# Performance work log

Measured on AMD Instinct MI355X. Metric: run time of the kernel, lower is better.

Reference implementation:

```python
import jax, jax.numpy as jnp
import numpy as np

D_MODEL = 512
NUM_HEADS = 8
DEPTH = D_MODEL // NUM_HEADS


def setup_inputs() -> dict:
    key = jax.random.key(0)
    ks = jax.random.split(key, 12)
    B, S, D = 2, 4096, D_MODEL
    scale = 1.0 / np.sqrt(D)
    return {
        "q": jax.random.normal(ks[0], (B, S, D), jnp.float32),
        "k": jax.random.normal(ks[1], (B, S, D), jnp.float32),
        "v": jax.random.normal(ks[2], (B, S, D), jnp.float32),
        "mask": jnp.zeros((B, 1, 1, S), jnp.float32),
        "wq": jax.random.normal(ks[3], (D, D), jnp.float32) * scale,
        "bq": jnp.zeros((D,), jnp.float32),
        "wk": jax.random.normal(ks[4], (D, D), jnp.float32) * scale,
        "bk": jnp.zeros((D,), jnp.float32),
        "wv": jax.random.normal(ks[5], (D, D), jnp.float32) * scale,
        "bv": jnp.zeros((D,), jnp.float32),
        "wo": jax.random.normal(ks[6], (D, D), jnp.float32) * scale,
        "bo": jnp.zeros((D,), jnp.float32),
    }


def _split_heads(x):
    # [B, S, D] -> [B, H, S, depth]
    B, S, _ = x.shape
    return x.reshape(B, S, NUM_HEADS, DEPTH).transpose(0, 2, 1, 3)


def reference(q, k, v, mask, wq, bq, wk, bk, wv, bv, wo, bo):
    B, S, D = q.shape
    query = _split_heads(q @ wq + bq)   # [B,H,S,d]
    key = _split_heads(k @ wk + bk)
    value = _split_heads(v @ wv + bv)
    # NOTE: original module does NOT scale by 1/sqrt(depth)
    score = jnp.einsum("bhqd,bhkd->bhqk", query, key)
    score = score + mask * -1e9
    attn = jax.nn.softmax(score, axis=-1)
    out = jnp.einsum("bhqk,bhkd->bhqd", attn, value)  # [B,H,S,d]
    out = out.transpose(0, 2, 1, 3).reshape(B, S, D)
    return out @ wo + bo
```

## Files before the change

kernel.cpp:

```cpp
#include <hip/hip_runtime.h>

#define NH   8
#define DH   64
#define NB   2
#define SEQ  4096
#define DM   512
#define MR   (NB * SEQ)
#define LSTR 72
#define LOG2E 1.44269504089f
#define NSPL 2
#define KVS  (SEQ / NSPL)
#define RH   (NB * NH * SEQ)

using f16x8 = __attribute__((ext_vector_type(8))) _Float16;
using f32x4 = __attribute__((ext_vector_type(4))) float;
using h2    = __attribute__((ext_vector_type(2))) _Float16;
#define MFMA16(a, b, c) __builtin_amdgcn_mfma_f32_16x16x32_f16(a, b, c, 0, 0, 0)

#if defined(__has_builtin) && __has_builtin(__builtin_amdgcn_exp2f)
#define EXP2(x) __builtin_amdgcn_exp2f(x)
#else
extern "C" __device__ float __ocml_native_exp2_f32(float);
#define EXP2(x) __ocml_native_exp2_f32(x)
#endif

__device__ __forceinline__ unsigned pk_f16(float a, float b) {
    typedef __fp16 fp16v2 __attribute__((ext_vector_type(2)));
    union { fp16v2 h; unsigned u; } c;
    c.h = __builtin_amdgcn_cvt_pkrtz(a, b);
    return c.u;
}
__device__ __forceinline__ unsigned sel_shfl(unsigned a, unsigned b, int pick, int src) {
    const unsigned va = __shfl(a, src);
    const unsigned vb = __shfl(b, src);
    return pick ? vb : va;
}
__device__ __forceinline__ float m3(float a, float b, float c) {
    return fmaxf(fmaxf(a, b), c);
}
__device__ __forceinline__ float dot2acc(unsigned u, float c) {
#if defined(__has_builtin) && __has_builtin(__builtin_amdgcn_fdot2)
    h2 a = __builtin_bit_cast(h2, u);
    h2 one = {(_Float16)1.f, (_Float16)1.f};
    return __builtin_amdgcn_fdot2(a, one, c, false);
#else
    h2 a = __builtin_bit_cast(h2, u);
    return c + (float)a[0] + (float)a[1];
#endif
}
__device__ __forceinline__ void async16(void* lds, const void* g) {
    __builtin_amdgcn_global_load_lds(
        (__attribute__((address_space(1))) void*)g,
        (__attribute__((address_space(3))) void*)lds, 16, 0, 0);
}

__global__ __launch_bounds__(256) void cvt_w(
    const float* __restrict__ w0, const float* __restrict__ w1,
    const float* __restrict__ w2, const float* __restrict__ w3,
    _Float16* __restrict__ Wt)
{
    __shared__ _Float16 T[64 * LSTR];
    const int z = blockIdx.z;
    const float* W = (z == 0) ? w0 : (z == 1 ? w1 : (z == 2 ? w2 : w3));
    _Float16* out = Wt + (size_t)z * DM * DM;
    const int t = threadIdx.x;
    const int k0 = blockIdx.x * 64, n0 = blockIdx.y * 64;
#pragma unroll
    for (int i = 0; i < 4; ++i) {
        const int kl  = i * 16 + (t >> 4);
        const int nl4 = (t & 15) * 4;
        float4 u = *(const float4*)(W + (size_t)(k0 + kl) * DM + n0 + nl4);
        T[(nl4 + 0) * LSTR + kl] = (_Float16)u.x;
        T[(nl4 + 1) * LSTR + kl] = (_Float16)u.y;
        T[(nl4 + 2) * LSTR + kl] = (_Float16)u.z;
        T[(nl4 + 3) * LSTR + kl] = (_Float16)u.w;
    }
    __syncthreads();
#pragma unroll
    for (int i = 0; i < 2; ++i) {
        const int nl = i * 32 + (t >> 3);
        const int kc = (t & 7) * 8;
        *(uint4*)(out + (size_t)(n0 + nl) * DM + k0 + kc) = *(const uint4*)&T[nl * LSTR + kc];
    }
}

__global__ __launch_bounds__(256) void maskprep(const float* __restrict__ mask,
                                                float* __restrict__ mw)
{
    const int i = blockIdx.x * 256 + threadIdx.x;
    mw[i] = mask[i] * (-1e9f * LOG2E);
}

__global__ __launch_bounds__(256) void cvt_qkv(
    const float* __restrict__ q, const float* __restrict__ k,
    const float* __restrict__ v,
    _Float16* __restrict__ Qo, _Float16* __restrict__ Ko, _Float16* __restrict__ Vo)
{
    const size_t PER = (size_t)MR * DM;
    size_t base = ((size_t)blockIdx.x * 256 + threadIdx.x) * 8;
    const int tz = (int)(base / PER);
    const size_t off = base % PER;
    const float* s = (tz == 0) ? q : (tz == 1 ? k : v);
    _Float16* d    = (tz == 0) ? Qo : (tz == 1 ? Ko : Vo);
    float4 a = *(const float4*)(s + off);
    float4 b = *(const float4*)(s + off + 4);
    uint4 p = make_uint4(pk_f16(a.x, a.y), pk_f16(a.z, a.w),
                         pk_f16(b.x, b.y), pk_f16(b.z, b.w));
    *(uint4*)(d + off) = p;
}

__global__ __launch_bounds__(256) void proj3(
    const _Float16* __restrict__ Qin, const _Float16* __restrict__ Kin,
    const _Float16* __restrict__ Vin, const _Float16* __restrict__ Wt,
    const float* __restrict__ bq, const float* __restrict__ bk,
    const float* __restrict__ bv,
    _Float16* __restrict__ Qo, _Float16* __restrict__ Ko,
    _Float16* __restrict__ VTo)
{
    __shared__ _Float16 Xs[2][128 * 64];
    __shared__ _Float16 Ws[2][64 * 64];

    const int z = blockIdx.z;
    const _Float16* X = (z == 0) ? Qin : (z == 1 ? Kin : Vin);
    const _Float16* W = Wt + (size_t)z * DM * DM;
    const float* bias = (z == 0) ? bq : (z == 1 ? bk : bv);
    const float scale = (z == 0) ? LOG2E : 1.0f;

    const int t = threadIdx.x;
    const int l = t & 63, w = t >> 6;
    const int m = l & 15, g = l >> 4;
    const int ms = m & 7;
    const int row0 = blockIdx.x * 128;
    const int col0 = blockIdx.y * 64;

    int xr[4], xsw[4];
#pragma unroll
    for (int i = 0; i < 4; ++i) {
        const int c = w * 256 + i * 64 + l;
        xr[i]  = c >> 3;
        xsw[i] = ((c & 7) ^ (xr[i] & 7)) * 8;
    }
    int wr[2], wsw[2];
#pragma unroll
    for (int i = 0; i < 2; ++i) {
        const int c = w * 128 + i * 64 + l;
        wr[i]  = c >> 3;
        wsw[i] = ((c & 7) ^ (wr[i] & 7)) * 8;
    }

#pragma unroll
    for (int i = 0; i < 4; ++i)
        async16(&Xs[0][(w * 256 + i * 64) * 8], X + (size_t)(row0 + xr[i]) * DM + xsw[i]);
#pragma unroll
    for (int i = 0; i < 2; ++i)
        async16(&Ws[0][(w * 128 + i * 64) * 8], W + (size_t)(col0 + wr[i]) * DM + wsw[i]);

    f32x4 acc[2][4] = {};

    for (int k0 = 0; k0 < DM; k0 += 64) {
        const int p = (k0 >> 6) & 1;
        __syncthreads();
        if (k0 + 64 < DM) {
            const int kn = k0 + 64;
#pragma unroll
            for (int i = 0; i < 4; ++i)
                async16(&Xs[p ^ 1][(w * 256 + i * 64) * 8],
                        X + (size_t)(row0 + xr[i]) * DM + kn + xsw[i]);
#pragma unroll
            for (int i = 0; i < 2; ++i)
                async16(&Ws[p ^ 1][(w * 128 + i * 64) * 8],
                        W + (size_t)(col0 + wr[i]) * DM + kn + wsw[i]);
        }
#pragma unroll
        for (int kk = 0; kk < 2; ++kk) {
            const int slot = ((kk * 4 + g) ^ ms) * 8;
            f16x8 a0 = *(const f16x8*)&Xs[p][(w * 32 + m) * 64 + slot];
            f16x8 a1 = *(const f16x8*)&Xs[p][(w * 32 + 16 + m) * 64 + slot];
#pragma unroll
            for (int ct = 0; ct < 4; ++ct) {
                f16x8 bf = *(const f16x8*)&Ws[p][(ct * 16 + m) * 64 + slot];
                acc[0][ct] = MFMA16(a0, bf, acc[0][ct]);
                acc[1][ct] = MFMA16(a1, bf, acc[1][ct]);
            }
        }
    }

    float bv4[4];
#pragma unroll
    for (int ct = 0; ct < 4; ++ct) bv4[ct] = bias[col0 + ct * 16 + m];

    if (z == 2) {
        __syncthreads();
        _Float16* T = &Xs[0][0];
#pragma unroll
        for (int rt = 0; rt < 2; ++rt)
#pragma unroll
            for (int reg = 0; reg < 4; ++reg) {
                const int s_l = w * 32 + rt * 16 + g * 4 + reg;
#pragma unroll
                for (int ct = 0; ct < 4; ++ct) {
                    const int d = ct * 16 + m;
                    T[d * 136 + s_l] = (_Float16)(acc[rt][ct][reg] + bv4[ct]);
                }
            }
        __syncthreads();
        const int bb = row0 >> 12;
        const int s0 = row0 & (SEQ - 1);
#pragma unroll
        for (int j = 0; j < 4; ++j) {
            const int c = j * 256 + t;
            const int d = c >> 4;
            const int sc = (c & 15) * 8;
            *(uint4*)(VTo + (((size_t)bb * NH + blockIdx.y) * DH + d) * SEQ + s0 + sc) =
                *(const uint4*)&T[d * 136 + sc];
        }
    } else {
        _Float16* out = (z == 0) ? Qo : Ko;
#pragma unroll
        for (int rt = 0; rt < 2; ++rt)
#pragma unroll
            for (int reg = 0; reg < 4; ++reg) {
                const int row = row0 + w * 32 + rt * 16 + g * 4 + reg;
                const int bb = row >> 12;
                const int s  = row & (SEQ - 1);
#pragma unroll
                for (int ct = 0; ct < 4; ++ct)
                    out[(((size_t)bb * NH + blockIdx.y) * SEQ + s) * DH + ct * 16 + m] =
                        (_Float16)(scale * (acc[rt][ct][reg] + bv4[ct]));
            }
    }
}

__global__ __launch_bounds__(256) void gemm_out(const _Float16* __restrict__ X,
                                                const _Float16* __restrict__ W,
                                                const float* __restrict__ bias,
                                                float* __restrict__ out)
{
    __shared__ _Float16 Xs[2][128 * 64];
    __shared__ _Float16 Ws[2][64 * 64];

    const int t = threadIdx.x;
    const int l = t & 63, w = t >> 6;
    const int m = l & 15, g = l >> 4;
    const int ms = m & 7;
    const int row0 = blockIdx.x * 128;
    const int col0 = blockIdx.y * 64;

    int xr[4], xsw[4];
#pragma unroll
    for (int i = 0; i < 4; ++i) {
        const int c = w * 256 + i * 64 + l;
        xr[i]  = c >> 3;
        xsw[i] = ((c & 7) ^ (xr[i] & 7)) * 8;
    }
    int wr[2], wsw[2];
#pragma unroll
    for (int i = 0; i < 2; ++i) {
        const int c = w * 128 + i * 64 + l;
        wr[i]  = c >> 3;
        wsw[i] = ((c & 7) ^ (wr[i] & 7)) * 8;
    }

#pragma unroll
    for (int i = 0; i < 4; ++i)
        async16(&Xs[0][(w * 256 + i * 64) * 8], X + (size_t)(row0 + xr[i]) * DM + xsw[i]);
#pragma unroll
    for (int i = 0; i < 2; ++i)
        async16(&Ws[0][(w * 128 + i * 64) * 8], W + (size_t)(col0 + wr[i]) * DM + wsw[i]);

    f32x4 acc[2][4] = {};

    for (int k0 = 0; k0 < DM; k0 += 64) {
        const int p = (k0 >> 6) & 1;
        __syncthreads();
        if (k0 + 64 < DM) {
            const int kn = k0 + 64;
#pragma unroll
            for (int i = 0; i < 4; ++i)
                async16(&Xs[p ^ 1][(w * 256 + i * 64) * 8],
                        X + (size_t)(row0 + xr[i]) * DM + kn + xsw[i]);
#pragma unroll
            for (int i = 0; i < 2; ++i)
                async16(&Ws[p ^ 1][(w * 128 + i * 64) * 8],
                        W + (size_t)(col0 + wr[i]) * DM + kn + wsw[i]);
        }
#pragma unroll
        for (int kk = 0; kk < 2; ++kk) {
            const int slot = ((kk * 4 + g) ^ ms) * 8;
            f16x8 a0 = *(const f16x8*)&Xs[p][(w * 32 + m) * 64 + slot];
            f16x8 a1 = *(const f16x8*)&Xs[p][(w * 32 + 16 + m) * 64 + slot];
#pragma unroll
            for (int ct = 0; ct < 4; ++ct) {
                f16x8 bf = *(const f16x8*)&Ws[p][(ct * 16 + m) * 64 + slot];
                acc[0][ct] = MFMA16(a0, bf, acc[0][ct]);
                acc[1][ct] = MFMA16(a1, bf, acc[1][ct]);
            }
        }
    }

    float bv4[4];
#pragma unroll
    for (int ct = 0; ct < 4; ++ct) bv4[ct] = bias[col0 + ct * 16 + m];

#pragma unroll
    for (int rt = 0; rt < 2; ++rt)
#pragma unroll
        for (int reg = 0; reg < 4; ++reg) {
            const int row = row0 + w * 32 + rt * 16 + g * 4 + reg;
#pragma unroll
            for (int ct = 0; ct < 4; ++ct)
                out[(size_t)row * DM + col0 + ct * 16 + m] = acc[rt][ct][reg] + bv4[ct];
        }
}

__global__ __launch_bounds__(256) void flash_mfma(
    const _Float16* __restrict__ Q, const _Float16* __restrict__ K,
    const _Float16* __restrict__ VT, const float* __restrict__ mw,
    _Float16* __restrict__ Op, float* __restrict__ Ml)
{
    __shared__ _Float16 Ks [2][64 * 64];
    __shared__ _Float16 VTs[2][64 * 64];

    const int t = threadIdx.x;
    const int l = t & 63, w = t >> 6;
    const int m = l & 15, g = l >> 4;
    const int bh = blockIdx.y;
    const int b  = bh >> 3;
    const int q0 = blockIdx.x * 128;
    const int z  = blockIdx.z;
    const int kb0 = z * KVS;

    const _Float16* Qh  = Q  + (size_t)bh * SEQ * DH;
    const _Float16* Kh  = K  + (size_t)bh * SEQ * DH;
    const _Float16* VTh = VT + (size_t)bh * DH * SEQ;
    const float* mwb = mw + (size_t)b * SEQ;

    const int c0 = w * 128 + l, c1 = c0 + 64;
    const int r0 = c0 >> 3,     r1 = c1 >> 3;
    const int cl0 = (c0 & 7) ^ (r0 & 7), cl1 = (c1 & 7) ^ (r1 & 7);
    const int    gK0 = r0 * DH + cl0 * 8, gK1 = r1 * DH + cl1 * 8;
    const size_t gV0 = (size_t)r0 * SEQ + cl0 * 8, gV1 = (size_t)r1 * SEQ + cl1 * 8;
    const int ldsA = w * 1024, ldsB = ldsA + 512;

    async16(&Ks[0][ldsA], Kh + (size_t)kb0 * DH + gK0);
    async16(&Ks[0][ldsB], Kh + (size_t)kb0 * DH + gK1);
    async16(&VTs[0][ldsA], VTh + kb0 + gV0);
    async16(&VTs[0][ldsB], VTh + kb0 + gV1);

    f16x8 qf[2][2];
#pragma unroll
    for (int h = 0; h < 2; ++h)
#pragma unroll
        for (int kk = 0; kk < 2; ++kk)
            qf[h][kk] = *(const f16x8*)(Qh + (size_t)(q0 + w * 32 + h * 16 + m) * DH +
                                        kk * 32 + g * 8);

    float m_r[2] = {-INFINITY, -INFINITY}, l_r[2] = {0.f, 0.f};
    f32x4 oacc[2][4] = {};

    const int srcA = m + (((g * 2) & 3) << 4);
    const int srcB = m + (((g * 2 + 1) & 3) << 4);
    const int pick = g >> 1;
    const int ms = m & 7;

    for (int it = 0; it < KVS / 64; ++it) {
        const int t0 = kb0 + it * 64;
        const int p  = it & 1;
        __syncthreads();

        if (it + 1 < KVS / 64) {
            const int tn = t0 + 64;
            async16(&Ks[p ^ 1][ldsA], Kh + (size_t)tn * DH + gK0);
            async16(&Ks[p ^ 1][ldsB], Kh + (size_t)tn * DH + gK1);
            async16(&VTs[p ^ 1][ldsA], VTh + tn + gV0);
            async16(&VTs[p ^ 1][ldsB], VTh + tn + gV1);
        }

        f32x4 sacc[2][4];
#pragma unroll
        for (int kt = 0; kt < 4; ++kt) {
            const f32x4 mv = *(const f32x4*)&mwb[t0 + kt * 16 + g * 4];
            sacc[0][kt] = mv;
            sacc[1][kt] = mv;
        }
#pragma unroll
        for (int kk = 0; kk < 2; ++kk) {
            const int slot = ((kk * 4 + g) ^ ms) * 8;
#pragma unroll
            for (int kt = 0; kt < 4; ++kt) {
                f16x8 kf = *(const f16x8*)&Ks[p][(kt * 16 + m) * 64 + slot];
                sacc[0][kt] = MFMA16(kf, qf[0][kk], sacc[0][kt]);
                sacc[1][kt] = MFMA16(kf, qf[1][kk], sacc[1][kt]);
            }
        }

        float rmax[2];
#pragma unroll
        for (int h = 0; h < 2; ++h) {
            const float x0 = m3(sacc[h][0][0], sacc[h][0][1], sacc[h][0][2]);
            const float x1 = m3(sacc[h][0][3], sacc[h][1][0], sacc[h][1][1]);
            const float x2 = m3(sacc[h][1][2], sacc[h][1][3], sacc[h][2][0]);
            const float x3 = m3(sacc[h][2][1], sacc[h][2][2], sacc[h][2][3]);
            const float x4 = m3(sacc[h][3][0], sacc[h][3][1], sacc[h][3][2]);
            float r = fmaxf(m3(x0, x1, x2), m3(x3, x4, sacc[h][3][3]));
            r = fmaxf(r, __shfl_xor(r, 16));
            r = fmaxf(r, __shfl_xor(r, 32));
            rmax[h] = r;
        }

        if (!__all(rmax[0] <= m_r[0] + 8.f && rmax[1] <= m_r[1] + 8.f)) {
#pragma unroll
            for (int h = 0; h < 2; ++h) {
                const float mnew  = fmaxf(m_r[h], rmax[h]);
                const float alpha = EXP2(m_r[h] - mnew);
                m_r[h] = mnew;
                l_r[h] *= alpha;
#pragma unroll
                for (int dt = 0; dt < 4; ++dt)
#pragma unroll
                    for (int r = 0; r < 4; ++r) oacc[h][dt][r] *= alpha;
            }
        }

        unsigned pkw[2][4][2];
#pragma unroll
        for (int h = 0; h < 2; ++h) {
            float ps0 = 0.f, ps1 = 0.f;
#pragma unroll
            for (int kt = 0; kt < 4; ++kt) {
                const float p0 = EXP2(sacc[h][kt][0] - m_r[h]);
                const float p1 = EXP2(sacc[h][kt][1] - m_r[h]);
                const float p2 = EXP2(sacc[h][kt][2] - m_r[h]);
                const float p3 = EXP2(sacc[h][kt][3] - m_r[h]);
                pkw[h][kt][0] = pk_f16(p0, p1);
                pkw[h][kt][1] = pk_f16(p2, p3);
                if (kt < 2) {
                    ps0 = dot2acc(pkw[h][kt][0], ps0);
                    ps0 = dot2acc(pkw[h][kt][1], ps0);
                } else {
                    ps1 = dot2acc(pkw[h][kt][0], ps1);
                    ps1 = dot2acc(pkw[h][kt][1], ps1);
                }
            }
            l_r[h] += ps0 + ps1;
        }

#pragma unroll
        for (int kk = 0; kk < 2; ++kk) {
            union { unsigned u[4]; f16x8 h; } pf[2];
#pragma unroll
            for (int h = 0; h < 2; ++h) {
                pf[h].u[0] = sel_shfl(pkw[h][2 * kk][0], pkw[h][2 * kk + 1][0], pick, srcA);
                pf[h].u[1] = sel_shfl(pkw[h][2 * kk][1], pkw[h][2 * kk + 1][1], pick, srcA);
                pf[h].u[2] = sel_shfl(pkw[h][2 * kk][0], pkw[h][2 * kk + 1][0], pick, srcB);
                pf[h].u[3] = sel_shfl(pkw[h][2 * kk][1], pkw[h][2 * kk + 1][1], pick, srcB);
            }
            const int slot = ((kk * 4 + g) ^ ms) * 8;
#pragma unroll
            for (int dt = 0; dt < 4; ++dt) {
                f16x8 vf = *(const f16x8*)&VTs[p][(dt * 16 + m) * 64 + slot];
                oacc[0][dt] = MFMA16(vf, pf[0].h, oacc[0][dt]);
                oacc[1][dt] = MFMA16(vf, pf[1].h, oacc[1][dt]);
            }
        }
    }

#pragma unroll
    for (int h = 0; h < 2; ++h) {
        float lv = l_r[h];
        lv += __shfl_xor(lv, 16);
        lv += __shfl_xor(lv, 32);
        const float inv = 1.0f / lv;
        const int q = q0 + w * 32 + h * 16 + m;
        const size_t rowi = ((size_t)z * NB * NH + bh) * SEQ + q;
        _Float16* Orow = Op + rowi * DH;
#pragma unroll
        for (int dt = 0; dt < 4; ++dt) {
            _Float16 o4[4] = { (_Float16)(oacc[h][dt][0] * inv),
                               (_Float16)(oacc[h][dt][1] * inv),
                               (_Float16)(oacc[h][dt][2] * inv),
                               (_Float16)(oacc[h][dt][3] * inv) };
            *(uint2*)(Orow + dt * 16 + g * 4) = *(const uint2*)o4;
        }
        if (g == 0) ((float2*)Ml)[rowi] = make_float2(m_r[h], lv);
    }
}

__global__ __launch_bounds__(256) void combine(const _Float16* __restrict__ Op,
                                               const float* __restrict__ Ml,
                                               _Float16* __restrict__ O)
{
    const int i = blockIdx.x * 256 + threadIdx.x;
    const int r = i >> 4;
    const int dq = (i & 15) * 4;
    const float2 ml0 = ((const float2*)Ml)[r];
    const float2 ml1 = ((const float2*)Ml)[RH + r];
    const float M = fmaxf(ml0.x, ml1.x);
    float a0 = EXP2(ml0.x - M) * ml0.y;
    float a1 = EXP2(ml1.x - M) * ml1.y;
    const float inv = 1.f / (a0 + a1);
    a0 *= inv; a1 *= inv;
    union { uint2 u; _Float16 h[4]; } v0, v1, o;
    v0.u = *(const uint2*)(Op + (size_t)r * DH + dq);
    v1.u = *(const uint2*)(Op + ((size_t)RH + r) * DH + dq);
#pragma unroll
    for (int j = 0; j < 4; ++j)
        o.h[j] = (_Float16)(a0 * (float)v0.h[j] + a1 * (float)v1.h[j]);
    const int bh = r >> 12, q = r & (SEQ - 1);
    const int b = bh >> 3, h = bh & 7;
    *(uint2*)(O + ((size_t)b * SEQ + q) * DM + h * DH + dq) = o.u;
}

extern "C" void kernel_launch(void* const* d_in, const int* in_sizes, int n_in,
                              void* d_out, int out_size, void* d_ws, size_t ws_size,
                              hipStream_t stream) {
    const float* q    = (const float*)d_in[0];
    const float* k    = (const float*)d_in[1];
    const float* v    = (const float*)d_in[2];
    const float* mask = (const float*)d_in[3];
    const float* wq   = (const float*)d_in[4];
    const float* bq   = (const float*)d_in[5];
    const float* wk   = (const float*)d_in[6];
    const float* bk   = (const float*)d_in[7];
    const float* wv   = (const float*)d_in[8];
    const float* bv   = (const float*)d_in[9];
    const float* wo   = (const float*)d_in[10];
    const float* bo   = (const float*)d_in[11];

    const size_t P8 = (size_t)MR * DM;
    _Float16* Wt  = (_Float16*)d_ws;
    float*    mw  = (float*)(Wt + (size_t)4 * DM * DM);
    _Float16* Qin = (_Float16*)(mw + NB * SEQ);
    _Float16* Kin = Qin + P8;
    _Float16* Vin = Kin + P8;
    _Float16* Qws = Vin + P8;
    _Float16* Kws = Qws + P8;
    _Float16* VTws = Kws + P8;
    _Float16* Ows  = VTws + P8;

    _Float16* Opart = Qin;
    float*    Mlb   = (float*)Vin;

    cvt_w<<<dim3(8, 8, 4), 256, 0, stream>>>(wq, wk, wv, wo, Wt);
    maskprep<<<dim3(NB * SEQ / 256), 256, 0, stream>>>(mask, mw);
    cvt_qkv<<<dim3(3 * (MR * DM / 8) / 256), 256, 0, stream>>>(q, k, v, Qin, Kin, Vin);

    proj3<<<dim3(MR / 128, DM / 64, 3), 256, 0, stream>>>(
        Qin, Kin, Vin, Wt, bq, bk, bv, Qws, Kws, VTws);

    flash_mfma<<<dim3(SEQ / 128, NB * NH, NSPL), 256, 0, stream>>>(
        Qws, Kws, VTws, mw, Opart, Mlb);

    combine<<<dim3(RH * 16 / 256), 256, 0, stream>>>(Opart, Mlb, Ows);

    gemm_out<<<dim3(MR / 128, DM / 64), 256, 0, stream>>>(
        Ows, Wt + (size_t)3 * DM * DM, bo, (float*)d_out);
}
```

Measured before the change: 289.5 us.

## Stage softmax P through per-wave LDS instead of lane shuffles; defer row-max reduction

Replaces the ds_bpermute-based relayout of the packed fp16 probabilities with a per-wave LDS staging buffer. Each lane writes its P values, then reads a 128-bit fragment in the layout the PV MFMA expects. The cross-lane row-max shuffles now run only inside the rare rescale branch; the skip test uses lane-local maxima. It also adds a minimum of 3 blocks per CU to launch_bounds. The trade is about 18KB of extra LDS per block and more LDS traffic, in exchange for fewer shuffles per tile.

```diff
diff --git a/kernel.cpp b/kernel.cpp
--- a/kernel.cpp
+++ b/kernel.cpp
@@ -11,6 +11,7 @@
 #define NSPL 2
 #define KVS  (SEQ / NSPL)
 #define RH   (NB * NH * SEQ)
+#define PSTR 36
 
 using f16x8 = __attribute__((ext_vector_type(8))) _Float16;
 using f32x4 = __attribute__((ext_vector_type(4))) float;
@@ -29,11 +30,6 @@
     union { fp16v2 h; unsigned u; } c;
     c.h = __builtin_amdgcn_cvt_pkrtz(a, b);
     return c.u;
-}
-__device__ __forceinline__ unsigned sel_shfl(unsigned a, unsigned b, int pick, int src) {
-    const unsigned va = __shfl(a, src);
-    const unsigned vb = __shfl(b, src);
-    return pick ? vb : va;
 }
 __device__ __forceinline__ float m3(float a, float b, float c) {
     return fmaxf(fmaxf(a, b), c);
@@ -313,13 +309,14 @@
         }
 }
 
-__global__ __launch_bounds__(256) void flash_mfma(
+__global__ __launch_bounds__(256, 3) void flash_mfma(
     const _Float16* __restrict__ Q, const _Float16* __restrict__ K,
     const _Float16* __restrict__ VT, const float* __restrict__ mw,
     _Float16* __restrict__ Op, float* __restrict__ Ml)
 {
     __shared__ _Float16 Ks [2][64 * 64];
     __shared__ _Float16 VTs[2][64 * 64];
+    __shared__ unsigned Ps[4][32 * PSTR];
 
     const int t = threadIdx.x;
     const int l = t & 63, w = t >> 6;
@@ -358,9 +355,7 @@
     float m_r[2] = {-INFINITY, -INFINITY}, l_r[2] = {0.f, 0.f};
     f32x4 oacc[2][4] = {};
 
-    const int srcA = m + (((g * 2) & 3) << 4);
-    const int srcB = m + (((g * 2 + 1) & 3) << 4);
-    const int pick = g >> 1;
+    unsigned* Pw = &Ps[w][0];
     const int ms = m & 7;
 
     for (int it = 0; it < KVS / 64; ++it) {
@@ -394,7 +389,7 @@
             }
         }
 
-        float rmax[2];
+        float lmax[2];
 #pragma unroll
         for (int h = 0; h < 2; ++h) {
             const float x0 = m3(sacc[h][0][0], sacc[h][0][1], sacc[h][0][2]);
@@ -402,29 +397,28 @@
             const float x2 = m3(sacc[h][1][2], sacc[h][1][3], sacc[h][2][0]);
             const float x3 = m3(sacc[h][2][1], sacc[h][2][2], sacc[h][2][3]);
             const float x4 = m3(sacc[h][3][0], sacc[h][3][1], sacc[h][3][2]);
-            float r = fmaxf(m3(x0, x1, x2), m3(x3, x4, sacc[h][3][3]));
-            r = fmaxf(r, __shfl_xor(r, 16));
-            r = fmaxf(r, __shfl_xor(r, 32));
-            rmax[h] = r;
-        }
-
-        if (!__all(rmax[0] <= m_r[0] + 8.f && rmax[1] <= m_r[1] + 8.f)) {
+            lmax[h] = fmaxf(m3(x0, x1, x2), m3(x3, x4, sacc[h][3][3]));
+        }
+
+        if (!__all(lmax[0] <= m_r[0] + 8.f && lmax[1] <= m_r[1] + 8.f)) {
 #pragma unroll
             for (int h = 0; h < 2; ++h) {
-                const float mnew  = fmaxf(m_r[h], rmax[h]);
+                float r = fmaxf(lmax[h], __shfl_xor(lmax[h], 16));
+                r = fmaxf(r, __shfl_xor(r, 32));
+                const float mnew  = fmaxf(m_r[h], r);
                 const float alpha = EXP2(m_r[h] - mnew);
                 m_r[h] = mnew;
                 l_r[h] *= alpha;
 #pragma unroll
                 for (int dt = 0; dt < 4; ++dt)
 #pragma unroll
-                    for (int r = 0; r < 4; ++r) oacc[h][dt][r] *= alpha;
-            }
-        }
-
-        unsigned pkw[2][4][2];
+                    for (int r4 = 0; r4 < 4; ++r4) oacc[h][dt][r4] *= alpha;
+            }
+        }
+
 #pragma unroll
         for (int h = 0; h < 2; ++h) {
+            const int pwr = (h * 16 + m) * PSTR + g * 2;
             float ps0 = 0.f, ps1 = 0.f;
 #pragma unroll
             for (int kt = 0; kt < 4; ++kt) {
@@ -432,14 +426,15 @@
                 const float p1 = EXP2(sacc[h][kt][1] - m_r[h]);
                 const float p2 = EXP2(sacc[h][kt][2] - m_r[h]);
                 const float p3 = EXP2(sacc[h][kt][3] - m_r[h]);
-                pkw[h][kt][0] = pk_f16(p0, p1);
-                pkw[h][kt][1] = pk_f16(p2, p3);
+                const unsigned u0 = pk_f16(p0, p1);
+                const unsigned u1 = pk_f16(p2, p3);
+                *(uint2*)&Pw[pwr + kt * 8] = make_uint2(u0, u1);
                 if (kt < 2) {
-                    ps0 = dot2acc(pkw[h][kt][0], ps0);
-                    ps0 = dot2acc(pkw[h][kt][1], ps0);
+                    ps0 = dot2acc(u0, ps0);
+                    ps0 = dot2acc(u1, ps0);
                 } else {
-                    ps1 = dot2acc(pkw[h][kt][0], ps1);
-                    ps1 = dot2acc(pkw[h][kt][1], ps1);
+                    ps1 = dot2acc(u0, ps1);
+                    ps1 = dot2acc(u1, ps1);
                 }
             }
             l_r[h] += ps0 + ps1;
@@ -447,14 +442,10 @@
 
 #pragma unroll
         for (int kk = 0; kk < 2; ++kk) {
-            union { unsigned u[4]; f16x8 h; } pf[2];
-#pragma unroll
-            for (int h = 0; h < 2; ++h) {
-                pf[h].u[0] = sel_shfl(pkw[h][2 * kk][0], pkw[h][2 * kk + 1][0], pick, srcA);
-                pf[h].u[1] = sel_shfl(pkw[h][2 * kk][1], pkw[h][2 * kk + 1][1], pick, srcA);
-                pf[h].u[2] = sel_shfl(pkw[h][2 * kk][0], pkw[h][2 * kk + 1][0], pick, srcB);
-                pf[h].u[3] = sel_shfl(pkw[h][2 * kk][1], pkw[h][2 * kk + 1][1], pick, srcB);
-            }
+            union { uint4 u4; f16x8 h; } pf[2];
+#pragma unroll
+            for (int h = 0; h < 2; ++h)
+                pf[h].u4 = *(const uint4*)&Pw[(h * 16 + m) * PSTR + kk * 16 + g * 4];
             const int slot = ((kk * 4 + g) ^ ms) * 8;
 #pragma unroll
             for (int dt = 0; dt < 4; ++dt) {
```

New measurement: 260.8 us. 1.11x faster.
